# Optimization experiments

Measured on AMD Instinct MI355X. Metric: run time of the kernel, lower is better.

## Reference

```python
import jax, jax.numpy as jnp
import numpy as np

N_NODES = 50000
N_EDGES = 600000
D = 128
HIDDEN = 128
OUT = 1


def setup_inputs() -> dict:
    key = jax.random.key(0)
    ks = jax.random.split(key, 6)
    z = jax.random.normal(ks[0], (N_NODES, D), dtype=jnp.float32)
    e = jax.random.randint(ks[1], (2, N_EDGES), 0, N_NODES, dtype=jnp.int64)
    # Linear weights in [in, out] layout; scaled like torch default init
    W1 = jax.random.normal(ks[2], (2 * D, HIDDEN), dtype=jnp.float32) / np.sqrt(2 * D)
    b1 = jax.random.normal(ks[3], (HIDDEN,), dtype=jnp.float32) / np.sqrt(2 * D)
    W2 = jax.random.normal(ks[4], (HIDDEN, OUT), dtype=jnp.float32) / np.sqrt(HIDDEN)
    b2 = jax.random.normal(ks[5], (OUT,), dtype=jnp.float32) / np.sqrt(HIDDEN)
    return {"z": z, "e": e, "W1": W1, "b1": b1, "W2": W2, "b2": b2}


def reference(z, e, W1, b1, W2, b2):
    x_i = z[e[0]]                      # [E, D] gather source nodes
    x_j = z[e[1]]                      # [E, D] gather target nodes
    x = jnp.concatenate([x_i, x_j], axis=1)  # [E, 2D]
    h = jax.nn.relu(x @ W1 + b1)       # [E, HIDDEN]
    out = h @ W2 + b2                  # [E, OUT]
    return jax.nn.sigmoid(out).squeeze()  # [E]
```

## Files before the change

kernel.cpp:

```cpp
#include <hip/hip_runtime.h>


#define DD 128

typedef __attribute__((ext_vector_type(8))) short short8;
typedef __attribute__((ext_vector_type(4))) float floatx4;

static __device__ __forceinline__ unsigned short f2bf(float f) {
  unsigned int u = __builtin_bit_cast(unsigned int, f);
  u += 0x7fffu + ((u >> 16) & 1u);
  return (unsigned short)(u >> 16);
}
static __device__ __forceinline__ float bflo(unsigned int u) {
  return __builtin_bit_cast(float, u << 16);
}
static __device__ __forceinline__ float bfhi(unsigned int u) {
  return __builtin_bit_cast(float, u & 0xffff0000u);
}

__global__ __launch_bounds__(256) void wt_build(
    const float* __restrict__ W1, unsigned short* __restrict__ Wt) {
  const int g = blockIdx.x * 256 + threadIdx.x;
  const int c = g >> 5;
  const int kq = (g & 31) * 4;
  const float* src = (c < 128) ? (W1 + c) : (W1 + 128 * 128 + (c - 128));
  ushort4 o;
  o.x = f2bf(src[(size_t)(kq + 0) * 128]);
  o.y = f2bf(src[(size_t)(kq + 1) * 128]);
  o.z = f2bf(src[(size_t)(kq + 2) * 128]);
  o.w = f2bf(src[(size_t)(kq + 3) * 128]);
  *(ushort4*)&Wt[c * 128 + kq] = o;
}

__global__ __launch_bounds__(256) void node_mfma(
    const float* __restrict__ z, const unsigned short* __restrict__ Wt,
    const float* __restrict__ b1, unsigned short* __restrict__ gi,
    unsigned short* __restrict__ gj, int n_nodes) {
  __shared__ unsigned short zb[128 * 136];
  const int tid = threadIdx.x;
  const int nb = blockIdx.x * 128;

#pragma unroll
  for (int i = 0; i < 16; ++i) {
    int q = tid + i * 256;
    int nl = q >> 5;
    int node = nb + nl; if (node >= n_nodes) node = n_nodes - 1;
    float4 v = ((const float4*)z)[(size_t)node * 32 + (q & 31)];
    ushort4 o;
    o.x = f2bf(v.x); o.y = f2bf(v.y); o.z = f2bf(v.z); o.w = f2bf(v.w);
    *(ushort4*)&zb[nl * 136 + (q & 31) * 4] = o;
  }
  __syncthreads();

  const int w = tid >> 6, lane = tid & 63;
  const int l15 = lane & 15, quad = lane >> 4;

  short8 a[2][4];
#pragma unroll
  for (int u = 0; u < 2; ++u)
#pragma unroll
    for (int s = 0; s < 4; ++s)
      a[u][s] = *(const short8*)&zb[(w * 32 + u * 16 + l15) * 136 + s * 32 + quad * 8];

  floatx4 acc[2][16];
#pragma unroll
  for (int t = 0; t < 16; ++t) {
    float bias = (t < 8) ? b1[t * 16 + l15] : 0.f;
    floatx4 b4 = {bias, bias, bias, bias};
    acc[0][t] = b4; acc[1][t] = b4;
  }

#pragma unroll
  for (int t = 0; t < 16; ++t) {
    const unsigned short* wrow = Wt + (size_t)(t * 16 + l15) * 128 + quad * 8;
#pragma unroll
    for (int s = 0; s < 4; ++s) {
      short8 b = *(const short8*)(wrow + s * 32);
      acc[0][t] = __builtin_amdgcn_mfma_f32_16x16x32_bf16(a[0][s], b, acc[0][t], 0, 0, 0);
      acc[1][t] = __builtin_amdgcn_mfma_f32_16x16x32_bf16(a[1][s], b, acc[1][t], 0, 0, 0);
    }
  }

#pragma unroll
  for (int u = 0; u < 2; ++u)
#pragma unroll
    for (int t = 0; t < 16; ++t) {
      unsigned short* base = (t < 8) ? gi : gj;
      const int cc = t * 16 + l15 - ((t < 8) ? 0 : 128);
#pragma unroll
      for (int r = 0; r < 4; ++r) {
        int node = nb + w * 32 + u * 16 + quad * 4 + r;
        if (node < n_nodes) base[(size_t)node * 128 + cc] = f2bf(acc[u][t][r]);
      }
    }
}

static __device__ __forceinline__ float dot8(uint4 a, uint4 b, float4 w0, float4 w1) {
  float s;
  s = fmaxf(bflo(a.x) + bflo(b.x), 0.f) * w0.x;
  s = fmaf(fmaxf(bfhi(a.x) + bfhi(b.x), 0.f), w0.y, s);
  s = fmaf(fmaxf(bflo(a.y) + bflo(b.y), 0.f), w0.z, s);
  s = fmaf(fmaxf(bfhi(a.y) + bfhi(b.y), 0.f), w0.w, s);
  s = fmaf(fmaxf(bflo(a.z) + bflo(b.z), 0.f), w1.x, s);
  s = fmaf(fmaxf(bfhi(a.z) + bfhi(b.z), 0.f), w1.y, s);
  s = fmaf(fmaxf(bflo(a.w) + bflo(b.w), 0.f), w1.z, s);
  s = fmaf(fmaxf(bfhi(a.w) + bfhi(b.w), 0.f), w1.w, s);
  return s;
}

__global__ __launch_bounds__(256) void edge_mlp(
    const int* __restrict__ e, const unsigned short* __restrict__ gi,
    const unsigned short* __restrict__ gj, const float* __restrict__ W2,
    const float* __restrict__ b2, float* __restrict__ out, int E) {
  __shared__ float w2s[128];
  if (threadIdx.x < 128) w2s[threadIdx.x] = W2[threadIdx.x];
  __syncthreads();
  const int lane = threadIdx.x & 63;
  const int gw   = (int)((blockIdx.x * 256u + threadIdx.x) >> 6);
  const int edge = gw * 8 + (lane >> 3);
  const int p    = lane & 7;
  float acc = 0.f;
  if (edge < E) {
    const int i = e[edge];
    const int j = e[E + edge];
    const uint4* pi = (const uint4*)(gi + (size_t)i * 128);
    const uint4* pj = (const uint4*)(gj + (size_t)j * 128);
    uint4 a0 = pi[p], a1 = pi[8 + p];
    uint4 c0 = pj[p], c1 = pj[8 + p];
    const float4* wv = (const float4*)w2s;
    acc = dot8(a0, c0, wv[p * 2], wv[p * 2 + 1]) +
          dot8(a1, c1, wv[16 + p * 2], wv[16 + p * 2 + 1]);
  }
  acc += __shfl_xor(acc, 1);
  acc += __shfl_xor(acc, 2);
  acc += __shfl_xor(acc, 4);
  if (edge < E && p == 0) {
    float x = acc + b2[0];
    out[edge] = 1.f / (1.f + __expf(-x));
  }
}

__global__ __launch_bounds__(256) void edge_direct(
    const int* __restrict__ e, const float* __restrict__ z,
    const float* __restrict__ W1, const float* __restrict__ b1,
    const float* __restrict__ W2, const float* __restrict__ b2,
    float* __restrict__ out, int E) {
  const int lane = threadIdx.x & 63;
  const int edge = (int)((blockIdx.x * 256u + threadIdx.x) >> 6);
  if (edge >= E) return;
  const int i = e[edge], j = e[E + edge];
  const float* zi = z + (size_t)i * 128;
  const float* zj = z + (size_t)j * 128;
  const int c0 = lane * 2;
  float h0 = b1[c0], h1 = b1[c0 + 1];
  for (int k = 0; k < 128; ++k) {
    float a = zi[k], b = zj[k];
    float2 wt = *(const float2*)&W1[(size_t)k * 128 + c0];
    float2 wb = *(const float2*)&W1[(size_t)(128 + k) * 128 + c0];
    h0 = fmaf(a, wt.x, h0); h1 = fmaf(a, wt.y, h1);
    h0 = fmaf(b, wb.x, h0); h1 = fmaf(b, wb.y, h1);
  }
  float s = fmaxf(h0, 0.f) * W2[c0] + fmaxf(h1, 0.f) * W2[c0 + 1];
#pragma unroll
  for (int off = 1; off < 64; off <<= 1) s += __shfl_xor(s, off);
  if (lane == 0) out[edge] = 1.f / (1.f + __expf(-(s + b2[0])));
}

extern "C" void kernel_launch(void* const* d_in, const int* in_sizes, int n_in,
                              void* d_out, int out_size, void* d_ws, size_t ws_size,
                              hipStream_t stream) {
  const float* z  = (const float*)d_in[0];
  const int*   e  = (const int*)d_in[1];
  const float* W1 = (const float*)d_in[2];
  const float* b1 = (const float*)d_in[3];
  const float* W2 = (const float*)d_in[4];
  const float* b2 = (const float*)d_in[5];
  float* out = (float*)d_out;
  const int n_nodes = in_sizes[0] / DD;
  const int E = in_sizes[1] / 2;

  const size_t g_bytes = (size_t)n_nodes * DD * sizeof(unsigned short);
  const size_t wt_bytes = 256 * 128 * sizeof(unsigned short);
  if (ws_size >= 2 * g_bytes + wt_bytes) {
    unsigned short* gi = (unsigned short*)d_ws;
    unsigned short* gj = (unsigned short*)((char*)d_ws + g_bytes);
    unsigned short* Wt = (unsigned short*)((char*)d_ws + 2 * g_bytes);
    wt_build<<<32, 256, 0, stream>>>(W1, Wt);
    node_mfma<<<(n_nodes + 127) / 128, 256, 0, stream>>>(z, Wt, b1, gi, gj, n_nodes);
    const int waves = (E + 7) / 8;
    edge_mlp<<<(waves + 3) / 4, 256, 0, stream>>>(e, gi, gj, W2, b2, out, E);
  } else {
    edge_direct<<<(E + 3) / 4, 256, 0, stream>>>(e, z, W1, b1, W2, b2, out, E);
  }
}
```

Before: 137.9 us.

## Restructure node MFMA tiling per wave and make edge kernel grid-stride

```diff
diff --git a/kernel.cpp b/kernel.cpp
--- a/kernel.cpp
+++ b/kernel.cpp
@@ -36,12 +36,12 @@
     const float* __restrict__ z, const unsigned short* __restrict__ Wt,
     const float* __restrict__ b1, unsigned short* __restrict__ gi,
     unsigned short* __restrict__ gj, int n_nodes) {
-  __shared__ unsigned short zb[128 * 136];
+  __shared__ unsigned short zb[64 * 136];
   const int tid = threadIdx.x;
-  const int nb = blockIdx.x * 128;
-
-#pragma unroll
-  for (int i = 0; i < 16; ++i) {
+  const int nb = blockIdx.x * 64;
+
+#pragma unroll
+  for (int i = 0; i < 8; ++i) {
     int q = tid + i * 256;
     int nl = q >> 5;
     int node = nb + nl; if (node >= n_nodes) node = n_nodes - 1;
@@ -50,49 +50,63 @@
     o.x = f2bf(v.x); o.y = f2bf(v.y); o.z = f2bf(v.z); o.w = f2bf(v.w);
     *(ushort4*)&zb[nl * 136 + (q & 31) * 4] = o;
   }
-  __syncthreads();
 
   const int w = tid >> 6, lane = tid & 63;
   const int l15 = lane & 15, quad = lane >> 4;
 
-  short8 a[2][4];
-#pragma unroll
-  for (int u = 0; u < 2; ++u)
+  short8 a[4][4];
+#pragma unroll
+  for (int tt = 0; tt < 4; ++tt) {
+    const unsigned short* wrow =
+        Wt + (size_t)((w * 4 + tt) * 16 + l15) * 128 + quad * 8;
+#pragma unroll
+    for (int s = 0; s < 4; ++s) a[tt][s] = *(const short8*)(wrow + s * 32);
+  }
+
+  floatx4 acc[4][4];
+#pragma unroll
+  for (int tt = 0; tt < 4; ++tt) {
+    floatx4 bias = {0.f, 0.f, 0.f, 0.f};
+    if (w < 2) {
+      float4 b4 = *(const float4*)&b1[(w * 4 + tt) * 16 + quad * 4];
+      bias[0] = b4.x; bias[1] = b4.y; bias[2] = b4.z; bias[3] = b4.w;
+    }
+#pragma unroll
+    for (int nt = 0; nt < 4; ++nt) acc[tt][nt] = bias;
+  }
+
+  __syncthreads();
+
+#pragma unroll
+  for (int nt = 0; nt < 4; ++nt) {
+    short8 bz[4];
 #pragma unroll
     for (int s = 0; s < 4; ++s)
-      a[u][s] = *(const short8*)&zb[(w * 32 + u * 16 + l15) * 136 + s * 32 + quad * 8];
-
-  floatx4 acc[2][16];
-#pragma unroll
-  for (int t = 0; t < 16; ++t) {
-    float bias = (t < 8) ? b1[t * 16 + l15] : 0.f;
-    floatx4 b4 = {bias, bias, bias, bias};
-    acc[0][t] = b4; acc[1][t] = b4;
-  }
-
-#pragma unroll
-  for (int t = 0; t < 16; ++t) {
-    const unsigned short* wrow = Wt + (size_t)(t * 16 + l15) * 128 + quad * 8;
-#pragma unroll
-    for (int s = 0; s < 4; ++s) {
-      short8 b = *(const short8*)(wrow + s * 32);
-      acc[0][t] = __builtin_amdgcn_mfma_f32_16x16x32_bf16(a[0][s], b, acc[0][t], 0, 0, 0);
-      acc[1][t] = __builtin_amdgcn_mfma_f32_16x16x32_bf16(a[1][s], b, acc[1][t], 0, 0, 0);
-    }
-  }
-
-#pragma unroll
-  for (int u = 0; u < 2; ++u)
-#pragma unroll
-    for (int t = 0; t < 16; ++t) {
-      unsigned short* base = (t < 8) ? gi : gj;
-      const int cc = t * 16 + l15 - ((t < 8) ? 0 : 128);
-#pragma unroll
-      for (int r = 0; r < 4; ++r) {
-        int node = nb + w * 32 + u * 16 + quad * 4 + r;
-        if (node < n_nodes) base[(size_t)node * 128 + cc] = f2bf(acc[u][t][r]);
+      bz[s] = *(const short8*)&zb[(nt * 16 + l15) * 136 + s * 32 + quad * 8];
+#pragma unroll
+    for (int tt = 0; tt < 4; ++tt)
+#pragma unroll
+      for (int s = 0; s < 4; ++s)
+        acc[tt][nt] =
+            __builtin_amdgcn_mfma_f32_16x16x32_bf16(a[tt][s], bz[s], acc[tt][nt], 0, 0, 0);
+  }
+
+  unsigned short* base = (w < 2) ? gi : gj;
+  const int cbase = w * 64 - ((w < 2) ? 0 : 128);
+#pragma unroll
+  for (int nt = 0; nt < 4; ++nt) {
+    const int node = nb + nt * 16 + l15;
+    if (node < n_nodes) {
+#pragma unroll
+      for (int tt = 0; tt < 4; ++tt) {
+        const int c = cbase + tt * 16 + quad * 4;
+        ushort4 o;
+        o.x = f2bf(acc[tt][nt][0]); o.y = f2bf(acc[tt][nt][1]);
+        o.z = f2bf(acc[tt][nt][2]); o.w = f2bf(acc[tt][nt][3]);
+        *(ushort4*)&base[(size_t)node * 128 + c] = o;
       }
     }
+  }
 }
 
 static __device__ __forceinline__ float dot8(uint4 a, uint4 b, float4 w0, float4 w1) {
@@ -112,31 +126,28 @@
     const int* __restrict__ e, const unsigned short* __restrict__ gi,
     const unsigned short* __restrict__ gj, const float* __restrict__ W2,
     const float* __restrict__ b2, float* __restrict__ out, int E) {
-  __shared__ float w2s[128];
-  if (threadIdx.x < 128) w2s[threadIdx.x] = W2[threadIdx.x];
-  __syncthreads();
-  const int lane = threadIdx.x & 63;
-  const int gw   = (int)((blockIdx.x * 256u + threadIdx.x) >> 6);
-  const int edge = gw * 8 + (lane >> 3);
-  const int p    = lane & 7;
-  float acc = 0.f;
-  if (edge < E) {
+  const int p = threadIdx.x & 7;
+  const float4* wv = (const float4*)W2;
+  const float4 w0 = wv[p * 2],      w1 = wv[p * 2 + 1];
+  const float4 w2 = wv[16 + p * 2], w3 = wv[16 + p * 2 + 1];
+  const float bias2 = b2[0];
+
+  const int stride = gridDim.x * 32;
+  for (int edge = blockIdx.x * 32 + (threadIdx.x >> 3); edge < E; edge += stride) {
     const int i = e[edge];
     const int j = e[E + edge];
     const uint4* pi = (const uint4*)(gi + (size_t)i * 128);
     const uint4* pj = (const uint4*)(gj + (size_t)j * 128);
     uint4 a0 = pi[p], a1 = pi[8 + p];
     uint4 c0 = pj[p], c1 = pj[8 + p];
-    const float4* wv = (const float4*)w2s;
-    acc = dot8(a0, c0, wv[p * 2], wv[p * 2 + 1]) +
-          dot8(a1, c1, wv[16 + p * 2], wv[16 + p * 2 + 1]);
-  }
-  acc += __shfl_xor(acc, 1);
-  acc += __shfl_xor(acc, 2);
-  acc += __shfl_xor(acc, 4);
-  if (edge < E && p == 0) {
-    float x = acc + b2[0];
-    out[edge] = 1.f / (1.f + __expf(-x));
+    float acc = dot8(a0, c0, w0, w1) + dot8(a1, c1, w2, w3);
+    acc += __shfl_xor(acc, 1);
+    acc += __shfl_xor(acc, 2);
+    acc += __shfl_xor(acc, 4);
+    if (p == 0) {
+      float x = acc + bias2;
+      out[edge] = 1.f / (1.f + __expf(-x));
+    }
   }
 }
 
@@ -186,9 +197,8 @@
     unsigned short* gj = (unsigned short*)((char*)d_ws + g_bytes);
     unsigned short* Wt = (unsigned short*)((char*)d_ws + 2 * g_bytes);
     wt_build<<<32, 256, 0, stream>>>(W1, Wt);
-    node_mfma<<<(n_nodes + 127) / 128, 256, 0, stream>>>(z, Wt, b1, gi, gj, n_nodes);
-    const int waves = (E + 7) / 8;
-    edge_mlp<<<(waves + 3) / 4, 256, 0, stream>>>(e, gi, gj, W2, b2, out, E);
+    node_mfma<<<(n_nodes + 63) / 64, 256, 0, stream>>>(z, Wt, b1, gi, gj, n_nodes);
+    edge_mlp<<<2048, 256, 0, stream>>>(e, gi, gj, W2, b2, out, E);
   } else {
     edge_direct<<<(E + 3) / 4, 256, 0, stream>>>(e, z, W1, b1, W2, b2, out, E);
   }
```

Measured after the change: 134.3 us. -2.6%, faster.
